# Kernel optimization log

Hardware: AMD Instinct MI355X
Metric: run time of the kernel (lower is better)

## Reference

```python
import jax, jax.numpy as jnp
import numpy as np

NUM_GROUPS = 8
EPS = 1e-5


def group_norm(x, scale, bias):
    # x: [b, c, h, w]; 8 groups, affine, eps=1e-5 (torch GroupNorm defaults)
    b, c, h, w = x.shape
    xg = x.reshape(b, NUM_GROUPS, c // NUM_GROUPS * h * w)
    mean = jnp.mean(xg, axis=-1, keepdims=True)
    var = jnp.var(xg, axis=-1, keepdims=True)
    xg = (xg - mean) * jax.lax.rsqrt(var + EPS)
    x = xg.reshape(b, c, h, w)
    return x * scale[None, :, None, None] + bias[None, :, None, None]


def conv1x1(x, w, bias):
    # 1x1 conv == per-pixel linear: x [b,c,h,w], w [c_out,c_in], bias [c_out]
    return jnp.einsum('oc,bchw->bohw', w, x) + bias[None, :, None, None]


def setup_inputs() -> dict:
    key = jax.random.key(0)
    ks = jax.random.split(key, 11)
    b, c, h, w = 8, 512, 32, 32
    init = 1.0 / np.sqrt(c)
    d = {
        'x': jax.random.normal(ks[0], (b, c, h, w), dtype=jnp.float32),
        'gn_scale': jnp.ones((c,), jnp.float32),
        'gn_bias': jnp.zeros((c,), jnp.float32),
        'wq': jax.random.uniform(ks[1], (c, c), jnp.float32, -init, init),
        'bq': jax.random.uniform(ks[2], (c,), jnp.float32, -init, init),
        'wk': jax.random.uniform(ks[3], (c, c), jnp.float32, -init, init),
        'bk': jax.random.uniform(ks[4], (c,), jnp.float32, -init, init),
        'wv': jax.random.uniform(ks[5], (c, c), jnp.float32, -init, init),
        'bv': jax.random.uniform(ks[6], (c,), jnp.float32, -init, init),
        'wproj': jax.random.uniform(ks[7], (c, c), jnp.float32, -init, init),
        'bproj': jax.random.uniform(ks[8], (c,), jnp.float32, -init, init),
    }
    return d


def reference(x, gn_scale, gn_bias, wq, bq, wk, bk, wv, bv, wproj, bproj):
    b, c, h, w = x.shape
    h_ = group_norm(x, gn_scale, gn_bias)
    q = conv1x1(h_, wq, bq).reshape(b, c, h * w)  # [b,c,hw]
    k = conv1x1(h_, wk, bk).reshape(b, c, h * w)
    v = conv1x1(h_, wv, bv).reshape(b, c, h * w)
    scale = 1.0 / np.sqrt(c).astype(np.float32)
    # scores[b,i,j] = sum_c q[b,c,i]*k[b,c,j]
    scores = jnp.einsum('bci,bcj->bij', q, k) * scale
    attn = jax.nn.softmax(scores, axis=2)  # softmax over j (keys)
    # h_[b,c,i] = sum_j v[b,c,j] * attn[b,i,j]
    out = jnp.einsum('bcj,bij->bci', v, attn).reshape(b, c, h, w)
    out = conv1x1(out, wproj, bproj)
    return x + out
```

## Files before the change

kernel.cpp:

```cpp
#include <hip/hip_runtime.h>
#include <hip/hip_bf16.h>

#define DI __device__ __forceinline__

typedef __bf16 bf16x8 __attribute__((ext_vector_type(8)));
typedef float f32x4 __attribute__((ext_vector_type(4)));

typedef const void __attribute__((address_space(1))) gas_t;
typedef void __attribute__((address_space(3))) las_t;

DI unsigned short f2bf(float f) {
    unsigned u = __builtin_bit_cast(unsigned, f);
    u += 0x7fffu + ((u >> 16) & 1u);
    return (unsigned short)(u >> 16);
}

template <int ROWS>
DI void stage_tile(const unsigned short* __restrict__ g, int ldK,
                   unsigned short* lds, int t) {
    int row_in = t >> 3;
    int kg = (t & 7) ^ (row_in & 7);
    const unsigned short* src = g + (size_t)row_in * ldK + kg * 8;
    unsigned short* dst = lds + ((t >> 6) << 9);
#pragma unroll
    for (int c = 0; c < ROWS / 32; ++c) {
        __builtin_amdgcn_global_load_lds(
            (gas_t*)(unsigned long long)(src + (size_t)c * 32 * ldK),
            (las_t*)(unsigned)(unsigned long long)(dst + c * 2048),
            16, 0, 0);
    }
}

DI void stage64(const unsigned short* __restrict__ g, int ldK,
                unsigned short* lds, int t) {
    int row = t >> 3;
    int kg = (t & 7) ^ (row & 7);
    __builtin_amdgcn_global_load_lds(
        (gas_t*)(unsigned long long)(g + (size_t)row * ldK + kg * 8),
        (las_t*)(unsigned)(unsigned long long)(lds + ((t >> 6) << 9)),
        16, 0, 0);
}

DI bf16x8 frag(const unsigned short* lds, int r, int kg) {
    return *(const bf16x8*)((const char*)lds + r * 128 + ((kg ^ (r & 7)) << 4));
}

template <int MR>
DI void compute_step(const unsigned short* As_, const unsigned short* Bs_,
                     f32x4 (&acc)[MR][4], int wm, int wn, int l15, int lks) {
#pragma unroll
    for (int kk = 0; kk < 2; ++kk) {
        bf16x8 a_[MR], b_[4];
#pragma unroll
        for (int m = 0; m < MR; ++m) a_[m] = frag(As_, wm + m * 16 + l15, kk * 4 + lks);
#pragma unroll
        for (int n = 0; n < 4; ++n) b_[n] = frag(Bs_, wn + n * 16 + l15, kk * 4 + lks);
#pragma unroll
        for (int m = 0; m < MR; ++m)
#pragma unroll
            for (int n = 0; n < 4; ++n)
                acc[m][n] = __builtin_amdgcn_mfma_f32_16x16x32_bf16(a_[m], b_[n], acc[m][n], 0, 0, 0);
    }
}

__global__ __launch_bounds__(512, 2) void attn_flash(
        const unsigned short* __restrict__ qT, const unsigned short* __restrict__ kT,
        const unsigned short* __restrict__ vN, unsigned short* __restrict__ OT) {
    __shared__ __align__(16) unsigned short Kb[8][4096];
    __shared__ __align__(16) unsigned short Vb[8][4096];
    __shared__ __align__(16) unsigned short Ps[2048];
    __shared__ float red[4][32];
    const int bx = blockIdx.x, t = threadIdx.x;
    const int b = bx & 7;
    const int i0 = (bx >> 3) << 5;
    const int lane = t & 63, w = t >> 6;
    const int l15 = lane & 15, lks = lane >> 4, rbase = lks * 4;
    const int iq = w & 1, jq = w >> 1;
    const size_t sH = (size_t)1024 * 512;
    const unsigned short* Qg = qT + sH * b;
    const unsigned short* Kg = kT + sH * b;
    const unsigned short* Vg = vN + sH * b;
    const float scale = 0.044194173824159216f;

    bf16x8 q[16];
    {
        const unsigned short* qrow = Qg + (size_t)(i0 + iq * 16 + l15) * 512 + lks * 8;
#pragma unroll
        for (int kk = 0; kk < 16; ++kk) q[kk] = *(const bf16x8*)(qrow + kk * 32);
    }

    f32x4 oacc[2][4];
#pragma unroll
    for (int m = 0; m < 2; ++m)
#pragma unroll
        for (int cq = 0; cq < 4; ++cq) oacc[m][cq] = (f32x4){0.f, 0.f, 0.f, 0.f};
    float rs[4] = {0.f, 0.f, 0.f, 0.f};

#pragma unroll
    for (int cc = 0; cc < 8; ++cc)
        stage64(Kg + cc * 64, 512, &Kb[cc][0], t);
    asm volatile("s_waitcnt vmcnt(0)" ::: "memory");
    __syncthreads();

    for (int j0 = 0; j0 < 1024; j0 += 64) {
#pragma unroll
        for (int cc = 0; cc < 8; ++cc)
            stage64(Vg + (size_t)cc * 64 * 1024 + j0, 1024, &Vb[cc][0], t);

        f32x4 e4 = (f32x4){0.f, 0.f, 0.f, 0.f};
#pragma unroll
        for (int kk = 0; kk < 16; ++kk) {
            bf16x8 kf = frag(&Kb[kk >> 1][0], jq * 16 + l15, ((kk & 1) << 2) | lks);
            e4 = __builtin_amdgcn_mfma_f32_16x16x32_bf16(q[kk], kf, e4, 0, 0, 0);
        }
        const int jcol = jq * 16 + l15;
#pragma unroll
        for (int jr = 0; jr < 4; ++jr) {
            float e = __expf(e4[jr] * scale);
            int irow = iq * 16 + rbase + jr;
            *(unsigned short*)((char*)Ps + irow * 128 +
                (((jcol >> 3) ^ (irow & 7)) << 4) + ((jcol & 7) << 1)) = f2bf(e);
            float p = e;
            p += __shfl_xor(p, 1); p += __shfl_xor(p, 2);
            p += __shfl_xor(p, 4); p += __shfl_xor(p, 8);
            rs[jr] += p;
        }
        asm volatile("s_waitcnt vmcnt(0)" ::: "memory");
        __syncthreads();

        if (j0 + 64 < 1024) {
#pragma unroll
            for (int cc = 0; cc < 8; ++cc)
                stage64(Kg + (size_t)(j0 + 64) * 512 + cc * 64, 512, &Kb[cc][0], t);
        }
#pragma unroll
        for (int kk2 = 0; kk2 < 2; ++kk2) {
            bf16x8 pf0 = frag(Ps, l15, kk2 * 4 + lks);
            bf16x8 pf1 = frag(Ps, 16 + l15, kk2 * 4 + lks);
#pragma unroll
            for (int cq = 0; cq < 4; ++cq) {
                bf16x8 vf = frag(&Vb[w][0], cq * 16 + l15, kk2 * 4 + lks);
                oacc[0][cq] = __builtin_amdgcn_mfma_f32_16x16x32_bf16(pf0, vf, oacc[0][cq], 0, 0, 0);
                oacc[1][cq] = __builtin_amdgcn_mfma_f32_16x16x32_bf16(pf1, vf, oacc[1][cq], 0, 0, 0);
            }
        }
        asm volatile("s_waitcnt vmcnt(0)" ::: "memory");
        __syncthreads();
    }

    if (l15 == 0) {
#pragma unroll
        for (int jr = 0; jr < 4; ++jr)
            red[jq][iq * 16 + rbase + jr] = rs[jr];
    }
    __syncthreads();
    unsigned short* Ob = OT + sH * b;
#pragma unroll
    for (int m = 0; m < 2; ++m) {
#pragma unroll
        for (int jr = 0; jr < 4; ++jr) {
            int il = m * 16 + rbase + jr;
            float inv = 1.f / (red[0][il] + red[1][il] + red[2][il] + red[3][il]);
#pragma unroll
            for (int cq = 0; cq < 4; ++cq)
                Ob[(size_t)(i0 + il) * 512 + w * 64 + cq * 16 + l15] =
                    f2bf(oacc[m][cq][jr] * inv);
        }
    }
}

template <int TM, int MODE, int PIPE>
DI void gemm_phase(unsigned short* AsB, unsigned short* BsB,
                   const unsigned short* __restrict__ A, const unsigned short* __restrict__ B,
                   const float* __restrict__ b0, const float* __restrict__ b1,
                   const float* __restrict__ b2,
                   void* __restrict__ C0, void* __restrict__ C1, void* __restrict__ C2,
                   const float* __restrict__ resid,
                   int M, int N, int K, size_t sA, size_t sB, size_t sC,
                   int bx, int t) {
    constexpr int MR = TM / 32;
    constexpr int ABUF = TM * 64;
    constexpr int BBUF = 128 * 64;
    int b = bx & 7;
    int tile = bx >> 3;
    int nTx = N >> 7;
    int tx = tile % nTx, ty = tile / nTx;
    int m0 = ty * TM, n0 = tx << 7;
    const unsigned short* Ag = A + sA * b + (size_t)m0 * K;
    const unsigned short* Bg = B + sB * b + (size_t)n0 * K;
    int lane = t & 63, wid = t >> 6;
    int wm = (wid >> 1) * (TM / 2), wn = (wid & 1) * 64;
    const int l15 = lane & 15, lks = lane >> 4;
    const int rbase = lks * 4;

    f32x4 acc[MR][4];
#pragma unroll
    for (int i = 0; i < MR; ++i)
#pragma unroll
        for (int j = 0; j < 4; ++j) acc[i][j] = (f32x4){0.f, 0.f, 0.f, 0.f};

    float bn4[4];
    if constexpr (MODE == 3) {
#pragma unroll
        for (int n = 0; n < 4; ++n) bn4[n] = b0[n0 + wn + n * 16 + l15];
    }

    if constexpr (PIPE == 0) {
        for (int k0 = 0; k0 < K; k0 += 64) {
            stage_tile<TM>(Ag + k0, K, AsB, t);
            stage_tile<128>(Bg + k0, K, BsB, t);
            asm volatile("s_waitcnt vmcnt(0)" ::: "memory");
            __syncthreads();
            compute_step<MR>(AsB, BsB, acc, wm, wn, l15, lks);
            __syncthreads();
        }
    } else {
        stage_tile<TM>(Ag, K, AsB, t);
        stage_tile<128>(Bg, K, BsB, t);
        asm volatile("s_waitcnt vmcnt(0)" ::: "memory");
        __syncthreads();
        int cur = 0;
        for (int k0 = 0; k0 < K; k0 += 64) {
            if (k0 + 64 < K) {
                stage_tile<TM>(Ag + k0 + 64, K, AsB + (cur ^ 1) * ABUF, t);
                stage_tile<128>(Bg + k0 + 64, K, BsB + (cur ^ 1) * BBUF, t);
            }
            compute_step<MR>(AsB + cur * ABUF, BsB + cur * BBUF, acc, wm, wn, l15, lks);
            if (k0 + 64 < K) {
                asm volatile("s_waitcnt vmcnt(0)" ::: "memory");
                __syncthreads();
            }
            cur ^= 1;
        }
    }

    const size_t cb = sC * b;
    if constexpr (MODE == 0) {
#pragma unroll
        for (int m = 0; m < MR; ++m) {
            int mgg = m0 + wm + m * 16 + rbase;
            int region = mgg >> 9;
            int local = mgg & 511;
            const float* bias = (region == 0) ? b0 : (region == 1) ? b1 : b2;
            float bv4[4];
#pragma unroll
            for (int j = 0; j < 4; ++j) bv4[j] = bias[local + j];
            if (region < 2) {
                unsigned short* Ct = (unsigned short*)(region == 0 ? C0 : C1) + cb;
#pragma unroll
                for (int n = 0; n < 4; ++n) {
                    int ng = n0 + wn + n * 16 + l15;
                    f32x4 v = acc[m][n];
                    ushort4 o;
                    o.x = f2bf(v[0] + bv4[0]); o.y = f2bf(v[1] + bv4[1]);
                    o.z = f2bf(v[2] + bv4[2]); o.w = f2bf(v[3] + bv4[3]);
                    *(ushort4*)&Ct[(size_t)ng * 512 + local] = o;
                }
            } else {
                unsigned short* Vb_ = (unsigned short*)C2 + cb;
#pragma unroll
                for (int n = 0; n < 4; ++n) {
                    int ng = n0 + wn + n * 16 + l15;
                    f32x4 v = acc[m][n];
#pragma unroll
                    for (int j = 0; j < 4; ++j)
                        Vb_[(size_t)(local + j) * 1024 + ng] = f2bf(v[j] + bv4[j]);
                }
            }
        }
    } else {
        float* Cf = (float*)C0 + cb;
#pragma unroll
        for (int m = 0; m < MR; ++m) {
            int mg = m0 + wm + m * 16 + rbase;
#pragma unroll
            for (int n = 0; n < 4; ++n) {
                int ng = n0 + wn + n * 16 + l15;
                f32x4 v = acc[m][n];
                const float* rp = resid + cb + (size_t)ng * M + mg;
                float4 o;
                o.x = v[0] + bn4[n] + rp[0]; o.y = v[1] + bn4[n] + rp[1];
                o.z = v[2] + bn4[n] + rp[2]; o.w = v[3] + bn4[n] + rp[3];
                *(float4*)&Cf[(size_t)ng * M + mg] = o;
            }
        }
    }
}

DI void stats_body(const float* __restrict__ x, float2* __restrict__ part,
                   float* red, int bx, int t) {
    int b = bx & 7, g = (bx >> 3) & 7, ch = bx >> 6;
    size_t base = ((size_t)b * 512 + g * 64 + ch * 8) * 1024;
    const float4* xp = (const float4*)(x + base);
    float s = 0.f, q = 0.f;
#pragma unroll
    for (int it = 0; it < 8; ++it) {
        float4 v = xp[it * 256 + t];
        s += (v.x + v.y) + (v.z + v.w);
        q += (v.x * v.x + v.y * v.y) + (v.z * v.z + v.w * v.w);
    }
#pragma unroll
    for (int o = 32; o; o >>= 1) { s += __shfl_xor(s, o); q += __shfl_xor(q, o); }
    int lane = t & 63, wid = t >> 6;
    if (!lane) { red[wid] = s; red[4 + wid] = q; }
    __syncthreads();
    if (t == 0)
        part[((b * 8 + g) * 8) + ch] =
            make_float2(red[0] + red[1] + red[2] + red[3],
                        red[4] + red[5] + red[6] + red[7]);
}

__global__ __launch_bounds__(256) void prep_kernel(const float* __restrict__ x,
                                                   float2* __restrict__ part,
                                                   const float* __restrict__ w0,
                                                   const float* __restrict__ w1,
                                                   const float* __restrict__ w2,
                                                   const float* __restrict__ w3,
                                                   unsigned short* __restrict__ wb) {
    __shared__ float red[8];
    int bx = blockIdx.x, t = threadIdx.x;
    if (bx < 512) {
        stats_body(x, part, red, bx, t);
    } else {
        int chunk = bx - 512;
        int w = chunk >> 8;
        const float* sp = (w == 0) ? w0 : (w == 1) ? w1 : (w == 2) ? w2 : w3;
        unsigned short* o = wb + (size_t)w * 262144;
        int idx = (chunk & 255) * 256 + t;
        float4 v = ((const float4*)sp)[idx];
        ushort4 r;
        r.x = f2bf(v.x); r.y = f2bf(v.y); r.z = f2bf(v.z); r.w = f2bf(v.w);
        ((ushort4*)o)[idx] = r;
    }
}

__global__ __launch_bounds__(256) void gn_applyT(const float* __restrict__ x,
                                                 const float2* __restrict__ part,
                                                 const float* __restrict__ gs,
                                                 const float* __restrict__ gb,
                                                 unsigned short* __restrict__ hT) {
    __shared__ unsigned short tile[128 * 66];
    int bx = blockIdx.x, t = threadIdx.x;
    int b = bx & 7, g = (bx >> 3) & 7, ic = bx >> 6;
    int bg = b * 8 + g;
    float s = 0.f, q = 0.f;
#pragma unroll
    for (int k = 0; k < 8; ++k) { float2 p = part[bg * 8 + k]; s += p.x; q += p.y; }
    float mean = s * (1.f / 65536.f);
    float var = q * (1.f / 65536.f) - mean * mean;
    float rstd = rsqrtf(var + 1e-5f);

    int i4 = t & 31, cq = t >> 5;
    size_t xbase = ((size_t)b * 512 + g * 64) * 1024 + ic * 128;
#pragma unroll
    for (int pass = 0; pass < 8; ++pass) {
        int c = pass * 8 + cq;
        float4 v = *(const float4*)&x[xbase + (size_t)c * 1024 + i4 * 4];
        int gc = g * 64 + c;
        float sc = gs[gc] * rstd, bi = gb[gc] - mean * sc;
        unsigned short* tp = &tile[(i4 * 4) * 66 + c];
        tp[0]   = f2bf(v.x * sc + bi);
        tp[66]  = f2bf(v.y * sc + bi);
        tp[132] = f2bf(v.z * sc + bi);
        tp[198] = f2bf(v.w * sc + bi);
    }
    __syncthreads();
    int i = t >> 1, h = t & 1;
    const unsigned short* tp2 = &tile[i * 66 + h * 32];
    unsigned short* op = &hT[(size_t)b * (1024 * 512) + (size_t)(ic * 128 + i) * 512 + g * 64 + h * 32];
#pragma unroll
    for (int cc = 0; cc < 4; ++cc) {
        unsigned short tmp[8];
#pragma unroll
        for (int j = 0; j < 8; ++j) tmp[j] = tp2[cc * 8 + j];
        *(uint4*)&op[cc * 8] = *(const uint4*)tmp;
    }
}

template <int TM, int MODE, int MINW, int PIPE>
__global__ __launch_bounds__(256, MINW) void gemm_bt(
        const unsigned short* __restrict__ A, const unsigned short* __restrict__ B,
        const float* __restrict__ b0, const float* __restrict__ b1,
        const float* __restrict__ b2,
        void* __restrict__ C0, void* __restrict__ C1, void* __restrict__ C2,
        const float* __restrict__ resid,
        int M, int N, int K, size_t sA, size_t sB, size_t sC) {
    constexpr int NBUF = PIPE ? 2 : 1;
    __shared__ __align__(16) unsigned short As[NBUF * TM * 64];
    __shared__ __align__(16) unsigned short Bs[NBUF * 128 * 64];
    gemm_phase<TM, MODE, PIPE>(As, Bs, A, B, b0, b1, b2, C0, C1, C2, resid,
                               M, N, K, sA, sB, sC, blockIdx.x, threadIdx.x);
}

extern "C" void kernel_launch(void* const* d_in, const int* in_sizes, int n_in,
                              void* d_out, int out_size, void* d_ws, size_t ws_size,
                              hipStream_t stream) {
    const float* x  = (const float*)d_in[0];
    const float* gs = (const float*)d_in[1];
    const float* gb = (const float*)d_in[2];
    const float* wq = (const float*)d_in[3];
    const float* bq = (const float*)d_in[4];
    const float* wk = (const float*)d_in[5];
    const float* bk = (const float*)d_in[6];
    const float* wv = (const float*)d_in[7];
    const float* bv = (const float*)d_in[8];
    const float* wp = (const float*)d_in[9];
    const float* bp = (const float*)d_in[10];
    float* out = (float*)d_out;

    char* ws = (char*)d_ws;
    const size_t MB = 1u << 20;
    unsigned short* hT = (unsigned short*)(ws + 0);
    unsigned short* wb = (unsigned short*)(ws + 8 * MB);
    unsigned short* qT = (unsigned short*)(ws + 10 * MB);
    unsigned short* kT = (unsigned short*)(ws + 18 * MB);
    unsigned short* vN = (unsigned short*)(ws + 26 * MB);
    unsigned short* OT = (unsigned short*)(ws + 34 * MB);
    float2* gnpart     = (float2*)(ws + 42 * MB);

    const unsigned short* wpb = wb + 3 * 262144;
    const size_t sH = 1024 * 512;

    prep_kernel<<<1536, 256, 0, stream>>>(x, gnpart, wq, wk, wv, wp, wb);
    gn_applyT<<<512, 256, 0, stream>>>(x, gnpart, gs, gb, hT);

    gemm_bt<128, 0, 3, 0><<<768, 256, 0, stream>>>(
        wb, hT, bq, bk, bv, qT, kT, vN, nullptr,
        1536, 1024, 512, 0, sH, sH);
    attn_flash<<<256, 512, 0, stream>>>(qT, kT, vN, OT);
    gemm_bt<64, 3, 2, 1><<<512, 256, 0, stream>>>(
        OT, wpb, bp, nullptr, nullptr, out, nullptr, nullptr, x,
        1024, 512, 512, sH, 0, sH);
}
```

Baseline: 88.56 us.

## Load V fragments directly from global into registers, dropping V LDS staging

The attention kernel no longer stages V tiles through shared memory. Each wave now loads its V MFMA fragments straight from global memory into registers, which frees 64KB of LDS, and the launch bound is raised to 4 blocks per SM to raise occupancy. The QK^T reduction is also split into two independent accumulators so consecutive MFMAs do not depend on each other. In exchange, the V loads are narrower and less coalesced, their latency is exposed inside the loop, and the tighter launch bound puts more pressure on registers.

```diff
diff --git a/kernel.cpp b/kernel.cpp
--- a/kernel.cpp
+++ b/kernel.cpp
@@ -63,11 +63,10 @@
     }
 }
 
-__global__ __launch_bounds__(512, 2) void attn_flash(
+__global__ __launch_bounds__(512, 4) void attn_flash(
         const unsigned short* __restrict__ qT, const unsigned short* __restrict__ kT,
         const unsigned short* __restrict__ vN, unsigned short* __restrict__ OT) {
     __shared__ __align__(16) unsigned short Kb[8][4096];
-    __shared__ __align__(16) unsigned short Vb[8][4096];
     __shared__ __align__(16) unsigned short Ps[2048];
     __shared__ float red[4][32];
     const int bx = blockIdx.x, t = threadIdx.x;
@@ -88,6 +87,7 @@
 #pragma unroll
         for (int kk = 0; kk < 16; ++kk) q[kk] = *(const bf16x8*)(qrow + kk * 32);
     }
+    const unsigned short* vrow = Vg + (size_t)(w * 64 + l15) * 1024;
 
     f32x4 oacc[2][4];
 #pragma unroll
@@ -103,16 +103,21 @@
     __syncthreads();
 
     for (int j0 = 0; j0 < 1024; j0 += 64) {
-#pragma unroll
-        for (int cc = 0; cc < 8; ++cc)
-            stage64(Vg + (size_t)cc * 64 * 1024 + j0, 1024, &Vb[cc][0], t);
-
-        f32x4 e4 = (f32x4){0.f, 0.f, 0.f, 0.f};
-#pragma unroll
-        for (int kk = 0; kk < 16; ++kk) {
-            bf16x8 kf = frag(&Kb[kk >> 1][0], jq * 16 + l15, ((kk & 1) << 2) | lks);
-            e4 = __builtin_amdgcn_mfma_f32_16x16x32_bf16(q[kk], kf, e4, 0, 0, 0);
-        }
+        bf16x8 vf0[4];
+#pragma unroll
+        for (int cq = 0; cq < 4; ++cq)
+            vf0[cq] = *(const bf16x8*)(vrow + (size_t)cq * 16 * 1024 + j0 + lks * 8);
+
+        f32x4 ea = (f32x4){0.f, 0.f, 0.f, 0.f};
+        f32x4 eb = (f32x4){0.f, 0.f, 0.f, 0.f};
+#pragma unroll
+        for (int kc = 0; kc < 8; ++kc) {
+            bf16x8 kf0 = frag(&Kb[kc][0], jq * 16 + l15, lks);
+            bf16x8 kf1 = frag(&Kb[kc][0], jq * 16 + l15, 4 + lks);
+            ea = __builtin_amdgcn_mfma_f32_16x16x32_bf16(q[kc * 2], kf0, ea, 0, 0, 0);
+            eb = __builtin_amdgcn_mfma_f32_16x16x32_bf16(q[kc * 2 + 1], kf1, eb, 0, 0, 0);
+        }
+        f32x4 e4 = ea + eb;
         const int jcol = jq * 16 + l15;
 #pragma unroll
         for (int jr = 0; jr < 4; ++jr) {
@@ -125,7 +130,6 @@
             p += __shfl_xor(p, 4); p += __shfl_xor(p, 8);
             rs[jr] += p;
         }
-        asm volatile("s_waitcnt vmcnt(0)" ::: "memory");
         __syncthreads();
 
         if (j0 + 64 < 1024) {
@@ -133,16 +137,24 @@
             for (int cc = 0; cc < 8; ++cc)
                 stage64(Kg + (size_t)(j0 + 64) * 512 + cc * 64, 512, &Kb[cc][0], t);
         }
-#pragma unroll
-        for (int kk2 = 0; kk2 < 2; ++kk2) {
-            bf16x8 pf0 = frag(Ps, l15, kk2 * 4 + lks);
-            bf16x8 pf1 = frag(Ps, 16 + l15, kk2 * 4 + lks);
-#pragma unroll
-            for (int cq = 0; cq < 4; ++cq) {
-                bf16x8 vf = frag(&Vb[w][0], cq * 16 + l15, kk2 * 4 + lks);
-                oacc[0][cq] = __builtin_amdgcn_mfma_f32_16x16x32_bf16(pf0, vf, oacc[0][cq], 0, 0, 0);
-                oacc[1][cq] = __builtin_amdgcn_mfma_f32_16x16x32_bf16(pf1, vf, oacc[1][cq], 0, 0, 0);
-            }
+        bf16x8 vf1[4];
+#pragma unroll
+        for (int cq = 0; cq < 4; ++cq)
+            vf1[cq] = *(const bf16x8*)(vrow + (size_t)cq * 16 * 1024 + j0 + 32 + lks * 8);
+
+#pragma unroll
+        for (int cq = 0; cq < 4; ++cq) {
+            bf16x8 pf0 = frag(Ps, l15, lks);
+            bf16x8 pf1 = frag(Ps, 16 + l15, lks);
+            oacc[0][cq] = __builtin_amdgcn_mfma_f32_16x16x32_bf16(pf0, vf0[cq], oacc[0][cq], 0, 0, 0);
+            oacc[1][cq] = __builtin_amdgcn_mfma_f32_16x16x32_bf16(pf1, vf0[cq], oacc[1][cq], 0, 0, 0);
+        }
+#pragma unroll
+        for (int cq = 0; cq < 4; ++cq) {
+            bf16x8 pf0 = frag(Ps, l15, 4 + lks);
+            bf16x8 pf1 = frag(Ps, 16 + l15, 4 + lks);
+            oacc[0][cq] = __builtin_amdgcn_mfma_f32_16x16x32_bf16(pf0, vf1[cq], oacc[0][cq], 0, 0, 0);
+            oacc[1][cq] = __builtin_amdgcn_mfma_f32_16x16x32_bf16(pf1, vf1[cq], oacc[1][cq], 0, 0, 0);
         }
         asm volatile("s_waitcnt vmcnt(0)" ::: "memory");
         __syncthreads();
```

Measured after the change: 145.7 us. 1.65x slower.

## Stage attention K/V through registers and coalesce QKV epilogue stores via LDS

Applied to the files above, without the earlier changes.

The attention kernel now loads K and V tiles into registers with plain global loads and writes them to LDS after the QK compute, instead of direct global-to-LDS loads. This overlaps the fetch latency with the score MFMAs and drops the explicit vmcnt waits. The QK MFMA chain is split into two independent accumulators to shorten dependency latency. The QKV GEMM epilogue now transposes each warp's tile through LDS so it can issue 16-byte coalesced global stores instead of scattered 2-byte and 8-byte writes. It also reverses tile order so the V region is scheduled first. The cost is more registers (16 uint4 per thread), which may reduce occupancy at 512 threads with 2 blocks per CU.

```diff
diff --git a/kernel.cpp b/kernel.cpp
--- a/kernel.cpp
+++ b/kernel.cpp
@@ -31,16 +31,6 @@
     }
 }
 
-DI void stage64(const unsigned short* __restrict__ g, int ldK,
-                unsigned short* lds, int t) {
-    int row = t >> 3;
-    int kg = (t & 7) ^ (row & 7);
-    __builtin_amdgcn_global_load_lds(
-        (gas_t*)(unsigned long long)(g + (size_t)row * ldK + kg * 8),
-        (las_t*)(unsigned)(unsigned long long)(lds + ((t >> 6) << 9)),
-        16, 0, 0);
-}
-
 DI bf16x8 frag(const unsigned short* lds, int r, int kg) {
     return *(const bf16x8*)((const char*)lds + r * 128 + ((kg ^ (r & 7)) << 4));
 }
@@ -60,6 +50,22 @@
 #pragma unroll
             for (int n = 0; n < 4; ++n)
                 acc[m][n] = __builtin_amdgcn_mfma_f32_16x16x32_bf16(a_[m], b_[n], acc[m][n], 0, 0, 0);
+    }
+}
+
+DI void rt_put4(unsigned short* rt, int row, int col, ushort4 v) {
+    *(ushort4*)((char*)rt + row * 128 + (((col >> 3) ^ (row & 7)) << 4) + ((col & 7) << 1)) = v;
+}
+DI void rt_put1(unsigned short* rt, int row, int col, unsigned short v) {
+    *(unsigned short*)((char*)rt + row * 128 + (((col >> 3) ^ (row & 7)) << 4) + ((col & 7) << 1)) = v;
+}
+DI void rt_flush(const unsigned short* rt, unsigned short* gdst, size_t gstride, int lane) {
+    int r = lane >> 3, g = lane & 7;
+#pragma unroll
+    for (int rr = 0; rr < 8; ++rr) {
+        int row = rr * 8 + r;
+        uint4 v = *(const uint4*)((const char*)rt + row * 128 + ((g ^ (row & 7)) << 4));
+        *(uint4*)&gdst[(size_t)row * gstride + g * 8] = v;
     }
 }
 
@@ -82,6 +88,10 @@
     const unsigned short* Vg = vN + sH * b;
     const float scale = 0.044194173824159216f;
 
+    const int srow = t >> 3;
+    const int skg = (t & 7) ^ (srow & 7);
+    const int sdst = srow * 128 + (t & 7) * 16;
+
     bf16x8 q[16];
     {
         const unsigned short* qrow = Qg + (size_t)(i0 + iq * 16 + l15) * 512 + lks * 8;
@@ -96,23 +106,39 @@
         for (int cq = 0; cq < 4; ++cq) oacc[m][cq] = (f32x4){0.f, 0.f, 0.f, 0.f};
     float rs[4] = {0.f, 0.f, 0.f, 0.f};
 
-#pragma unroll
-    for (int cc = 0; cc < 8; ++cc)
-        stage64(Kg + cc * 64, 512, &Kb[cc][0], t);
-    asm volatile("s_waitcnt vmcnt(0)" ::: "memory");
+    {
+        uint4 k0r[8];
+#pragma unroll
+        for (int cc = 0; cc < 8; ++cc)
+            k0r[cc] = *(const uint4*)(Kg + (size_t)srow * 512 + cc * 64 + skg * 8);
+#pragma unroll
+        for (int cc = 0; cc < 8; ++cc)
+            *(uint4*)((char*)&Kb[cc][0] + sdst) = k0r[cc];
+    }
     __syncthreads();
 
     for (int j0 = 0; j0 < 1024; j0 += 64) {
+        const int jn = j0 + 64;
+        uint4 vreg[8], kreg[8];
 #pragma unroll
         for (int cc = 0; cc < 8; ++cc)
-            stage64(Vg + (size_t)cc * 64 * 1024 + j0, 1024, &Vb[cc][0], t);
-
-        f32x4 e4 = (f32x4){0.f, 0.f, 0.f, 0.f};
-#pragma unroll
-        for (int kk = 0; kk < 16; ++kk) {
-            bf16x8 kf = frag(&Kb[kk >> 1][0], jq * 16 + l15, ((kk & 1) << 2) | lks);
-            e4 = __builtin_amdgcn_mfma_f32_16x16x32_bf16(q[kk], kf, e4, 0, 0, 0);
-        }
+            vreg[cc] = *(const uint4*)(Vg + (size_t)(cc * 64 + srow) * 1024 + j0 + skg * 8);
+        if (jn < 1024) {
+#pragma unroll
+            for (int cc = 0; cc < 8; ++cc)
+                kreg[cc] = *(const uint4*)(Kg + (size_t)(jn + srow) * 512 + cc * 64 + skg * 8);
+        }
+
+        f32x4 ea = (f32x4){0.f, 0.f, 0.f, 0.f};
+        f32x4 eb = (f32x4){0.f, 0.f, 0.f, 0.f};
+#pragma unroll
+        for (int kc = 0; kc < 8; ++kc) {
+            bf16x8 kf0 = frag(&Kb[kc][0], jq * 16 + l15, lks);
+            bf16x8 kf1 = frag(&Kb[kc][0], jq * 16 + l15, 4 + lks);
+            ea = __builtin_amdgcn_mfma_f32_16x16x32_bf16(q[kc * 2], kf0, ea, 0, 0, 0);
+            eb = __builtin_amdgcn_mfma_f32_16x16x32_bf16(q[kc * 2 + 1], kf1, eb, 0, 0, 0);
+        }
+        f32x4 e4 = ea + eb;
         const int jcol = jq * 16 + l15;
 #pragma unroll
         for (int jr = 0; jr < 4; ++jr) {
@@ -125,14 +151,11 @@
             p += __shfl_xor(p, 4); p += __shfl_xor(p, 8);
             rs[jr] += p;
         }
-        asm volatile("s_waitcnt vmcnt(0)" ::: "memory");
+#pragma unroll
+        for (int cc = 0; cc < 8; ++cc)
+            *(uint4*)((char*)&Vb[cc][0] + sdst) = vreg[cc];
         __syncthreads();
 
-        if (j0 + 64 < 1024) {
-#pragma unroll
-            for (int cc = 0; cc < 8; ++cc)
-                stage64(Kg + (size_t)(j0 + 64) * 512 + cc * 64, 512, &Kb[cc][0], t);
-        }
 #pragma unroll
         for (int kk2 = 0; kk2 < 2; ++kk2) {
             bf16x8 pf0 = frag(Ps, l15, kk2 * 4 + lks);
@@ -144,7 +167,11 @@
                 oacc[1][cq] = __builtin_amdgcn_mfma_f32_16x16x32_bf16(pf1, vf, oacc[1][cq], 0, 0, 0);
             }
         }
-        asm volatile("s_waitcnt vmcnt(0)" ::: "memory");
+        if (jn < 1024) {
+#pragma unroll
+            for (int cc = 0; cc < 8; ++cc)
+                *(uint4*)((char*)&Kb[cc][0] + sdst) = kreg[cc];
+        }
         __syncthreads();
     }
 
@@ -185,6 +212,7 @@
     int tile = bx >> 3;
     int nTx = N >> 7;
     int tx = tile % nTx, ty = tile / nTx;
+    if constexpr (MODE == 0) ty = 11 - ty;
     int m0 = ty * TM, n0 = tx << 7;
     const unsigned short* Ag = A + sA * b + (size_t)m0 * K;
     const unsigned short* Bg = B + sB * b + (size_t)n0 * K;
@@ -236,37 +264,48 @@
 
     const size_t cb = sC * b;
     if constexpr (MODE == 0) {
-#pragma unroll
-        for (int m = 0; m < MR; ++m) {
-            int mgg = m0 + wm + m * 16 + rbase;
-            int region = mgg >> 9;
-            int local = mgg & 511;
-            const float* bias = (region == 0) ? b0 : (region == 1) ? b1 : b2;
-            float bv4[4];
-#pragma unroll
-            for (int j = 0; j < 4; ++j) bv4[j] = bias[local + j];
-            if (region < 2) {
-                unsigned short* Ct = (unsigned short*)(region == 0 ? C0 : C1) + cb;
+        __syncthreads();
+        unsigned short* rt = (wid < 2) ? (AsB + wid * 4096) : (BsB + (wid - 2) * 4096);
+        int region = m0 >> 9;
+        int local0 = m0 & 511;
+        if (region < 2) {
+            const float* bias = (region == 0) ? b0 : b1;
+#pragma unroll
+            for (int m = 0; m < MR; ++m) {
+                int cl = m * 16 + rbase;
+                float bv4[4];
+#pragma unroll
+                for (int j = 0; j < 4; ++j) bv4[j] = bias[local0 + wm + cl + j];
 #pragma unroll
                 for (int n = 0; n < 4; ++n) {
-                    int ng = n0 + wn + n * 16 + l15;
                     f32x4 v = acc[m][n];
                     ushort4 o;
                     o.x = f2bf(v[0] + bv4[0]); o.y = f2bf(v[1] + bv4[1]);
                     o.z = f2bf(v[2] + bv4[2]); o.w = f2bf(v[3] + bv4[3]);
-                    *(ushort4*)&Ct[(size_t)ng * 512 + local] = o;
+                    rt_put4(rt, n * 16 + l15, cl, o);
                 }
-            } else {
-                unsigned short* Vb_ = (unsigned short*)C2 + cb;
+            }
+            unsigned short* Ct = (unsigned short*)(region == 0 ? C0 : C1) + cb
+                                 + (size_t)(n0 + wn) * 512 + local0 + wm;
+            rt_flush(rt, Ct, 512, lane);
+        } else {
+#pragma unroll
+            for (int m = 0; m < MR; ++m) {
+                float bv4[4];
+#pragma unroll
+                for (int j = 0; j < 4; ++j) bv4[j] = b2[local0 + wm + m * 16 + rbase + j];
 #pragma unroll
                 for (int n = 0; n < 4; ++n) {
-                    int ng = n0 + wn + n * 16 + l15;
+                    int cl = n * 16 + l15;
                     f32x4 v = acc[m][n];
 #pragma unroll
                     for (int j = 0; j < 4; ++j)
-                        Vb_[(size_t)(local + j) * 1024 + ng] = f2bf(v[j] + bv4[j]);
+                        rt_put1(rt, m * 16 + rbase + j, cl, f2bf(v[j] + bv4[j]));
                 }
             }
+            unsigned short* Vbp = (unsigned short*)C2 + cb
+                                  + (size_t)(local0 + wm) * 1024 + (n0 + wn);
+            rt_flush(rt, Vbp, 1024, lane);
         }
     } else {
         float* Cf = (float*)C0 + cb;
```

Result: slower. 137.1 us (+54.8%).
